# Performance work log

Hardware: AMD Instinct MI355X
Metric: run time of the kernel (lower is better)

## Reference

```python
import jax, jax.numpy as jnp
import numpy as np

N_NODES = 100_000
N_EDGES = 3_200_000
IN_CH = 128
HID = 128


def setup_inputs() -> dict:
    key = jax.random.key(0)
    k1, k2, k3, k4, k5 = jax.random.split(key, 5)
    x = jax.random.normal(k1, (N_NODES, IN_CH), dtype=jnp.float32)
    edge_index = jax.random.randint(k2, (2, N_EDGES), 0, N_NODES, dtype=jnp.int64)
    # GCNConv params: glorot-style weights, zero bias (as in PyG defaults)
    s1 = 1.0 / np.sqrt(IN_CH)
    s2 = 1.0 / np.sqrt(HID)
    W1 = jax.random.uniform(k3, (IN_CH, HID), jnp.float32, -s1, s1)
    b1 = jnp.zeros((HID,), jnp.float32)
    W2 = jax.random.uniform(k4, (HID, HID), jnp.float32, -s2, s2)
    b2 = jnp.zeros((HID,), jnp.float32)
    return {"x": x, "edge_index": edge_index, "W1": W1, "b1": b1, "W2": W2, "b2": b2}


def _gcn_conv(x, src, dst, W, b):
    """PyG GCNConv: add self-loops, symmetric D^-1/2 (A+I) D^-1/2 norm,
    linear transform first, then aggregate, then bias."""
    n = x.shape[0]
    loops = jnp.arange(n, dtype=src.dtype)
    s = jnp.concatenate([src, loops])          # [E+N]
    d = jnp.concatenate([dst, loops])          # [E+N]
    w = jnp.ones(s.shape[0], dtype=x.dtype)    # edge_weight=None -> ones
    deg = jax.ops.segment_sum(w, d, num_segments=n)            # [N]
    dinv = jnp.where(deg > 0, jax.lax.rsqrt(deg), 0.0)         # deg^-1/2
    norm = dinv[s] * w * dinv[d]                                # [E+N]
    xw = x @ W                                                  # [N, H]
    msg = xw[s] * norm[:, None]                                 # [E+N, H] gather
    out = jax.ops.segment_sum(msg, d, num_segments=n)           # [N, H] scatter
    return out + b


def reference(x, edge_index, W1, b1, W2, b2):
    src, dst = edge_index[0], edge_index[1]
    h1 = jax.nn.relu(_gcn_conv(x, src, dst, W1, b1))
    h2 = jax.nn.relu(_gcn_conv(h1, src, dst, W2, b2))
    return jnp.concatenate([h1, h2], axis=1)   # [N, 2*HID]
```

## Files before the change

### kernel.cpp

```cpp
#include <hip/hip_runtime.h>
#include <hip/hip_bf16.h>
#include <stdint.h>

#define NN 100000
#define BSH 9
#define BSZ 512
#define NBUCK 196
#define CAP 24576

static __device__ __forceinline__ float bf_lo(unsigned int u) {
    union { unsigned int i; float f; } c; c.i = u << 16; return c.f;
}
static __device__ __forceinline__ float bf_hi(unsigned int u) {
    union { unsigned int i; float f; } c; c.i = u & 0xffff0000u; return c.f;
}
static __device__ __forceinline__ unsigned short f2bf(float f) {
    union { float f; unsigned int i; } c; c.f = f;
    unsigned int r = (c.i + 0x7fffu + ((c.i >> 16) & 1u)) >> 16;
    return (unsigned short)r;
}

__global__ void k_init(int* __restrict__ gcursor, unsigned int* __restrict__ xwb_row_nn) {
    int i = threadIdx.x;
    if (i < NBUCK) gcursor[i] = i * CAP;
    if (i < 64) xwb_row_nn[i] = 0u;
}

__global__ __launch_bounds__(256) void k_bucket(const int* __restrict__ eb, int E,
                                                int* __restrict__ gcursor,
                                                unsigned int* __restrict__ pairs) {
    __shared__ int hist[NBUCK];
    __shared__ int gbase[NBUCK];
    __shared__ int shflag;
    int t = threadIdx.x;
    if (t < 64) {
        int v = eb[2 * t + 1];
        unsigned long long m = __ballot(v == 0);
        if (t == 0) shflag = (m == ~0ull) ? 1 : 0;
    }
    for (int i = t; i < NBUCK; i += 256) hist[i] = 0;
    __syncthreads();
    int sh = shflag;
    size_t base = (size_t)blockIdx.x * 4096;
    int srcs[16], rank[16], bks[16], dls[16];
#pragma unroll
    for (int k = 0; k < 16; k++) {
        size_t e = base + (size_t)k * 256 + t;
        if (e < (size_t)E) {
            int s = eb[e << sh];
            int d = eb[((size_t)E + e) << sh];
            int b = d >> BSH;
            srcs[k] = s; bks[k] = b; dls[k] = d & (BSZ - 1);
            rank[k] = atomicAdd(&hist[b], 1);
        } else {
            bks[k] = -1;
        }
    }
    __syncthreads();
    for (int i = t; i < NBUCK; i += 256) {
        int c = hist[i];
        gbase[i] = (c > 0) ? atomicAdd(&gcursor[i], c) : 0;
    }
    __syncthreads();
#pragma unroll
    for (int k = 0; k < 16; k++) {
        if (bks[k] >= 0) {
            int pos = gbase[bks[k]] + rank[k];
            if (pos < (bks[k] + 1) * CAP)
                pairs[pos] = ((unsigned int)dls[k] << 17) | (unsigned int)srcs[k];
        }
    }
}

__global__ __launch_bounds__(256) void k_pass2(const unsigned int* __restrict__ pairs,
                                               const int* __restrict__ gcursor,
                                               int* __restrict__ csr, int* __restrict__ ptr,
                                               int* __restrict__ degv, float* __restrict__ dinv) {
    __shared__ int hist2[BSZ * 8];
    __shared__ int cur2[BSZ * 8];
    __shared__ int hist[BSZ];
    __shared__ int lofs[BSZ];
    __shared__ int scanw[256];
    __shared__ int lcsr[CAP];
    int b = blockIdx.x, t = threadIdx.x;
    int base = b * CAP;
    int cnt = gcursor[b] - base;
    if (cnt > CAP) cnt = CAP;
    for (int i = t; i < BSZ * 8; i += 256) hist2[i] = 0;
    __syncthreads();
    for (int i = t; i < cnt; i += 256) {
        unsigned int p = pairs[base + i];
        int key = (int)((p >> 17) << 3) | (int)((p & 0x1FFFFu) >> 14);
        atomicAdd(&hist2[key], 1);
    }
    __syncthreads();
    int dl0 = 2 * t, dl1 = 2 * t + 1;
    int h0 = 0, h1 = 0;
#pragma unroll
    for (int oc = 0; oc < 8; oc++) { h0 += hist2[(dl0 << 3) | oc]; h1 += hist2[(dl1 << 3) | oc]; }
    hist[dl0] = h0; hist[dl1] = h1;
    int a = h0 + h1;
    scanw[t] = a;
    __syncthreads();
    for (int d = 1; d < 256; d <<= 1) {
        int x = (t >= d) ? scanw[t - d] : 0;
        __syncthreads();
        scanw[t] += x;
        __syncthreads();
    }
    int excl = scanw[t] - a;
    lofs[dl0] = excl;
    lofs[dl1] = excl + h0;
    int run = excl;
#pragma unroll
    for (int oc = 0; oc < 8; oc++) { cur2[(dl0 << 3) | oc] = run; run += hist2[(dl0 << 3) | oc]; }
#pragma unroll
    for (int oc = 0; oc < 8; oc++) { cur2[(dl1 << 3) | oc] = run; run += hist2[(dl1 << 3) | oc]; }
    __syncthreads();
    for (int i = t; i < cnt; i += 256) {
        unsigned int p = pairs[base + i];
        int src = (int)(p & 0x1FFFFu);
        int key = (int)((p >> 17) << 3) | (src >> 14);
        int pos = atomicAdd(&cur2[key], 1);
        lcsr[pos] = src;
    }
    __syncthreads();
    for (int i = t; i < cnt; i += 256) csr[base + i] = lcsr[i];
    int n0 = b << BSH;
    for (int g = t; g < BSZ; g += 256) {
        int n = n0 + g;
        if (n < NN) {
            int dg = hist[g];
            degv[n] = dg;
            ptr[n] = base + lofs[g];
            dinv[n] = rsqrtf((float)(dg + 1));
        }
    }
}

__global__ __launch_bounds__(256) void k_gemm(const float* __restrict__ A, int lda,
                                              const float* __restrict__ W,
                                              const float* __restrict__ dinv,
                                              unsigned short* __restrict__ outb, int M) {
    __shared__ float Wl[32 * 128];
    __shared__ float Al[64 * 33];
    int t = threadIdx.x;
    int row0 = blockIdx.x * 64;
    int cg = t & 15, rg = t >> 4;
    int c0 = cg * 8, r0 = rg * 4;
    float acc[4][8];
#pragma unroll
    for (int i = 0; i < 4; i++)
#pragma unroll
        for (int j = 0; j < 8; j++) acc[i][j] = 0.f;

    for (int kb = 0; kb < 4; kb++) {
        __syncthreads();
        const float4* Wg = (const float4*)(W + kb * 32 * 128);
        float4* Wl4 = (float4*)Wl;
#pragma unroll
        for (int i = 0; i < 4; i++) Wl4[t + 256 * i] = Wg[t + 256 * i];
#pragma unroll
        for (int i = 0; i < 2; i++) {
            int idx = t + 256 * i;
            int r = idx >> 3, c4 = idx & 7;
            int grow = row0 + r;
            float4 v = make_float4(0.f, 0.f, 0.f, 0.f);
            if (grow < M) v = *(const float4*)(A + (size_t)grow * lda + kb * 32 + c4 * 4);
            float* dp = &Al[r * 33 + c4 * 4];
            dp[0] = v.x; dp[1] = v.y; dp[2] = v.z; dp[3] = v.w;
        }
        __syncthreads();
#pragma unroll 8
        for (int k = 0; k < 32; k++) {
            float wv[8];
            *(float4*)&wv[0] = *(const float4*)&Wl[k * 128 + c0];
            *(float4*)&wv[4] = *(const float4*)&Wl[k * 128 + c0 + 4];
            float av[4];
#pragma unroll
            for (int i = 0; i < 4; i++) av[i] = Al[(r0 + i) * 33 + k];
#pragma unroll
            for (int i = 0; i < 4; i++)
#pragma unroll
                for (int j = 0; j < 8; j++)
                    acc[i][j] = fmaf(av[i], wv[j], acc[i][j]);
        }
    }
#pragma unroll
    for (int i = 0; i < 4; i++) {
        int grow = row0 + r0 + i;
        if (grow < M) {
            float dv = dinv[grow];
            unsigned int w[4];
#pragma unroll
            for (int j = 0; j < 4; j++)
                w[j] = (unsigned int)f2bf(acc[i][2 * j] * dv) |
                       ((unsigned int)f2bf(acc[i][2 * j + 1] * dv) << 16);
            uint4 pk = make_uint4(w[0], w[1], w[2], w[3]);
            *(uint4*)(outb + (size_t)grow * 128 + c0) = pk;
        }
    }
}

__global__ __launch_bounds__(256) void k_aggr(const unsigned short* __restrict__ xwb,
                                              const int* __restrict__ csr, const int* __restrict__ ptr,
                                              const int* __restrict__ degv,
                                              const float* __restrict__ dinv, const float* __restrict__ bias,
                                              float* __restrict__ outf, int N) {
    int wid = (blockIdx.x * 256 + threadIdx.x) >> 6;
    int lane = threadIdx.x & 63;
    if (wid >= N) return;
    int n = wid;
    int st = ptr[n];
    int en = st + degv[n];
    const unsigned short* xl = xwb + (lane << 1);
    float acc0 = 0.f, acc1 = 0.f;
    for (int j = st; j < en; j += 64) {
        int e = j + lane;
        int sp = (e < en) ? csr[e] : NN;
        int cnt = en - j; if (cnt > 64) cnt = 64;
        int cntr = (cnt + 7) & ~7;
        for (int q = 0; q < cntr; q += 8) {
            int s0 = __shfl(sp, q),     s1 = __shfl(sp, q + 1);
            int s2 = __shfl(sp, q + 2), s3 = __shfl(sp, q + 3);
            int s4 = __shfl(sp, q + 4), s5 = __shfl(sp, q + 5);
            int s6 = __shfl(sp, q + 6), s7 = __shfl(sp, q + 7);
            unsigned int u0 = *(const unsigned int*)(xl + ((size_t)s0 << 7));
            unsigned int u1 = *(const unsigned int*)(xl + ((size_t)s1 << 7));
            unsigned int u2 = *(const unsigned int*)(xl + ((size_t)s2 << 7));
            unsigned int u3 = *(const unsigned int*)(xl + ((size_t)s3 << 7));
            unsigned int u4 = *(const unsigned int*)(xl + ((size_t)s4 << 7));
            unsigned int u5 = *(const unsigned int*)(xl + ((size_t)s5 << 7));
            unsigned int u6 = *(const unsigned int*)(xl + ((size_t)s6 << 7));
            unsigned int u7 = *(const unsigned int*)(xl + ((size_t)s7 << 7));
            acc0 += bf_lo(u0); acc1 += bf_hi(u0);
            acc0 += bf_lo(u1); acc1 += bf_hi(u1);
            acc0 += bf_lo(u2); acc1 += bf_hi(u2);
            acc0 += bf_lo(u3); acc1 += bf_hi(u3);
            acc0 += bf_lo(u4); acc1 += bf_hi(u4);
            acc0 += bf_lo(u5); acc1 += bf_hi(u5);
            acc0 += bf_lo(u6); acc1 += bf_hi(u6);
            acc0 += bf_lo(u7); acc1 += bf_hi(u7);
        }
    }
    {
        unsigned int u = *(const unsigned int*)(xl + ((size_t)n << 7));
        acc0 += bf_lo(u);
        acc1 += bf_hi(u);
    }
    float dn = dinv[n];
    float2 bv = *(const float2*)(bias + (lane << 1));
    float o0 = fmaxf(fmaf(acc0, dn, bv.x), 0.f);
    float o1 = fmaxf(fmaf(acc1, dn, bv.y), 0.f);
    *(float2*)(outf + (size_t)n * 256 + (lane << 1)) = make_float2(o0, o1);
}

extern "C" void kernel_launch(void* const* d_in, const int* in_sizes, int n_in,
                              void* d_out, int out_size, void* d_ws, size_t ws_size,
                              hipStream_t stream) {
    const float* x  = (const float*)d_in[0];
    const int*   eb = (const int*)d_in[1];
    const float* W1 = (const float*)d_in[2];
    const float* b1 = (const float*)d_in[3];
    const float* W2 = (const float*)d_in[4];
    const float* b2 = (const float*)d_in[5];
    float* out = (float*)d_out;

    int E = in_sizes[1] / 2;

    char* w = (char*)d_ws;
    size_t o = 0;
    auto carve = [&](size_t bytes) { char* p = w + o; o += (bytes + 255) & ~(size_t)255; return p; };
    int*   gcursor = (int*)carve((size_t)NBUCK * 4);
    int*   ptr     = (int*)carve((size_t)NN * 4);
    int*   deg     = (int*)carve((size_t)NN * 4);
    float* dinv    = (float*)carve((size_t)NN * 4);
    int*   csr     = (int*)carve((size_t)NBUCK * CAP * 4);
    size_t big = (size_t)(NN + 1) * 128 * 2;
    size_t pb  = (size_t)NBUCK * CAP * 4;
    char* shared_region = carve(big > pb ? big : pb);
    unsigned int*   pairs = (unsigned int*)shared_region;
    unsigned short* xwb   = (unsigned short*)shared_region;
    (void)ws_size;

    int EB4 = (E + 4095) / 4096;
    int GB  = (NN + 63) / 64;
    int AB  = (NN + 3) / 4;

    k_init<<<1, 256, 0, stream>>>(gcursor, (unsigned int*)(xwb + (size_t)NN * 128));
    k_bucket<<<EB4, 256, 0, stream>>>(eb, E, gcursor, pairs);
    k_pass2<<<NBUCK, 256, 0, stream>>>(pairs, gcursor, csr, ptr, deg, dinv);

    k_gemm<<<GB, 256, 0, stream>>>(x, 128, W1, dinv, xwb, NN);
    k_aggr<<<AB, 256, 0, stream>>>(xwb, csr, ptr, deg, dinv, b1, out, NN);

    k_gemm<<<GB, 256, 0, stream>>>(out, 256, W2, dinv, xwb, NN);
    k_aggr<<<AB, 256, 0, stream>>>(xwb, csr, ptr, deg, dinv, b2, out + 128, NN);
}
```

Before: 528.8 us.

## Vectorize aggregation gathers to 16-byte loads and widen pass2 blocks

The aggregation kernel now splits each wavefront into four 16-lane groups. Each group gathers a full 256-byte bf16 row with uint4 loads, two neighbours per step, and the four partial sums are combined with cross-lane xor shuffles. Output is written with nontemporal vector stores. This replaces 4-byte-per-lane gathers with wider loads to cut per-edge memory instructions, at the cost of an extra reduction and idle lanes in the epilogue. Separately, the CSR build kernel runs with 1024 threads per block so the 196 buckets use more parallelism per block.

```diff
diff --git a/kernel.cpp b/kernel.cpp
--- a/kernel.cpp
+++ b/kernel.cpp
@@ -7,6 +7,8 @@
 #define BSZ 512
 #define NBUCK 196
 #define CAP 24576
+
+typedef float vfloat4 __attribute__((ext_vector_type(4)));
 
 static __device__ __forceinline__ float bf_lo(unsigned int u) {
     union { unsigned int i; float f; } c; c.i = u << 16; return c.f;
@@ -72,52 +74,52 @@
     }
 }
 
-__global__ __launch_bounds__(256) void k_pass2(const unsigned int* __restrict__ pairs,
-                                               const int* __restrict__ gcursor,
-                                               int* __restrict__ csr, int* __restrict__ ptr,
-                                               int* __restrict__ degv, float* __restrict__ dinv) {
+__global__ __launch_bounds__(1024) void k_pass2(const unsigned int* __restrict__ pairs,
+                                                const int* __restrict__ gcursor,
+                                                int* __restrict__ csr, int* __restrict__ ptr,
+                                                int* __restrict__ degv, float* __restrict__ dinv) {
     __shared__ int hist2[BSZ * 8];
     __shared__ int cur2[BSZ * 8];
     __shared__ int hist[BSZ];
     __shared__ int lofs[BSZ];
-    __shared__ int scanw[256];
+    __shared__ int scanw[BSZ];
     __shared__ int lcsr[CAP];
     int b = blockIdx.x, t = threadIdx.x;
     int base = b * CAP;
     int cnt = gcursor[b] - base;
     if (cnt > CAP) cnt = CAP;
-    for (int i = t; i < BSZ * 8; i += 256) hist2[i] = 0;
-    __syncthreads();
-    for (int i = t; i < cnt; i += 256) {
+    for (int i = t; i < BSZ * 8; i += 1024) hist2[i] = 0;
+    __syncthreads();
+    for (int i = t; i < cnt; i += 1024) {
         unsigned int p = pairs[base + i];
         int key = (int)((p >> 17) << 3) | (int)((p & 0x1FFFFu) >> 14);
         atomicAdd(&hist2[key], 1);
     }
     __syncthreads();
-    int dl0 = 2 * t, dl1 = 2 * t + 1;
-    int h0 = 0, h1 = 0;
-#pragma unroll
-    for (int oc = 0; oc < 8; oc++) { h0 += hist2[(dl0 << 3) | oc]; h1 += hist2[(dl1 << 3) | oc]; }
-    hist[dl0] = h0; hist[dl1] = h1;
-    int a = h0 + h1;
-    scanw[t] = a;
-    __syncthreads();
-    for (int d = 1; d < 256; d <<= 1) {
-        int x = (t >= d) ? scanw[t - d] : 0;
+    int h = 0;
+    if (t < BSZ) {
+#pragma unroll
+        for (int oc = 0; oc < 8; oc++) h += hist2[(t << 3) | oc];
+        scanw[t] = h;
+        hist[t] = h;
+    }
+    __syncthreads();
+    for (int d = 1; d < BSZ; d <<= 1) {
+        int x = 0;
+        if (t < BSZ && t >= d) x = scanw[t - d];
         __syncthreads();
-        scanw[t] += x;
+        if (t < BSZ) scanw[t] += x;
         __syncthreads();
     }
-    int excl = scanw[t] - a;
-    lofs[dl0] = excl;
-    lofs[dl1] = excl + h0;
-    int run = excl;
-#pragma unroll
-    for (int oc = 0; oc < 8; oc++) { cur2[(dl0 << 3) | oc] = run; run += hist2[(dl0 << 3) | oc]; }
-#pragma unroll
-    for (int oc = 0; oc < 8; oc++) { cur2[(dl1 << 3) | oc] = run; run += hist2[(dl1 << 3) | oc]; }
-    __syncthreads();
-    for (int i = t; i < cnt; i += 256) {
+    if (t < BSZ) {
+        int excl = scanw[t] - h;
+        lofs[t] = excl;
+        int run = excl;
+#pragma unroll
+        for (int oc = 0; oc < 8; oc++) { cur2[(t << 3) | oc] = run; run += hist2[(t << 3) | oc]; }
+    }
+    __syncthreads();
+    for (int i = t; i < cnt; i += 1024) {
         unsigned int p = pairs[base + i];
         int src = (int)(p & 0x1FFFFu);
         int key = (int)((p >> 17) << 3) | (src >> 14);
@@ -125,14 +127,14 @@
         lcsr[pos] = src;
     }
     __syncthreads();
-    for (int i = t; i < cnt; i += 256) csr[base + i] = lcsr[i];
+    for (int i = t; i < cnt; i += 1024) csr[base + i] = lcsr[i];
     int n0 = b << BSH;
-    for (int g = t; g < BSZ; g += 256) {
-        int n = n0 + g;
+    if (t < BSZ) {
+        int n = n0 + t;
         if (n < NN) {
-            int dg = hist[g];
+            int dg = hist[t];
             degv[n] = dg;
-            ptr[n] = base + lofs[g];
+            ptr[n] = base + lofs[t];
             dinv[n] = rsqrtf((float)(dg + 1));
         }
     }
@@ -211,48 +213,61 @@
     int lane = threadIdx.x & 63;
     if (wid >= N) return;
     int n = wid;
+    int g  = lane >> 4;
+    int sl = lane & 15;
     int st = ptr[n];
     int en = st + degv[n];
-    const unsigned short* xl = xwb + (lane << 1);
-    float acc0 = 0.f, acc1 = 0.f;
+    const uint4* xq = (const uint4*)xwb + sl;
+    float acc[8] = {0.f, 0.f, 0.f, 0.f, 0.f, 0.f, 0.f, 0.f};
     for (int j = st; j < en; j += 64) {
         int e = j + lane;
         int sp = (e < en) ? csr[e] : NN;
         int cnt = en - j; if (cnt > 64) cnt = 64;
         int cntr = (cnt + 7) & ~7;
         for (int q = 0; q < cntr; q += 8) {
-            int s0 = __shfl(sp, q),     s1 = __shfl(sp, q + 1);
-            int s2 = __shfl(sp, q + 2), s3 = __shfl(sp, q + 3);
-            int s4 = __shfl(sp, q + 4), s5 = __shfl(sp, q + 5);
-            int s6 = __shfl(sp, q + 6), s7 = __shfl(sp, q + 7);
-            unsigned int u0 = *(const unsigned int*)(xl + ((size_t)s0 << 7));
-            unsigned int u1 = *(const unsigned int*)(xl + ((size_t)s1 << 7));
-            unsigned int u2 = *(const unsigned int*)(xl + ((size_t)s2 << 7));
-            unsigned int u3 = *(const unsigned int*)(xl + ((size_t)s3 << 7));
-            unsigned int u4 = *(const unsigned int*)(xl + ((size_t)s4 << 7));
-            unsigned int u5 = *(const unsigned int*)(xl + ((size_t)s5 << 7));
-            unsigned int u6 = *(const unsigned int*)(xl + ((size_t)s6 << 7));
-            unsigned int u7 = *(const unsigned int*)(xl + ((size_t)s7 << 7));
-            acc0 += bf_lo(u0); acc1 += bf_hi(u0);
-            acc0 += bf_lo(u1); acc1 += bf_hi(u1);
-            acc0 += bf_lo(u2); acc1 += bf_hi(u2);
-            acc0 += bf_lo(u3); acc1 += bf_hi(u3);
-            acc0 += bf_lo(u4); acc1 += bf_hi(u4);
-            acc0 += bf_lo(u5); acc1 += bf_hi(u5);
-            acc0 += bf_lo(u6); acc1 += bf_hi(u6);
-            acc0 += bf_lo(u7); acc1 += bf_hi(u7);
-        }
-    }
-    {
-        unsigned int u = *(const unsigned int*)(xl + ((size_t)n << 7));
-        acc0 += bf_lo(u);
-        acc1 += bf_hi(u);
-    }
-    float dn = dinv[n];
-    float2 bv = *(const float2*)(bias + (lane << 1));
-    float o0 = fmaxf(fmaf(acc0, dn, bv.x), 0.f);
-    float o1 = fmaxf(fmaf(acc1, dn, bv.y), 0.f);
-    *(float2*)(outf + (size_t)n * 256 + (lane << 1)) = make_float2(o0, o1);
+            int s0 = __shfl(sp, q + g);
+            int s1 = __shfl(sp, q + 4 + g);
+            uint4 u0 = xq[(size_t)s0 * 16];
+            uint4 u1 = xq[(size_t)s1 * 16];
+            acc[0] += bf_lo(u0.x); acc[1] += bf_hi(u0.x);
+            acc[2] += bf_lo(u0.y); acc[3] += bf_hi(u0.y);
+            acc[4] += bf_lo(u0.z); acc[5] += bf_hi(u0.z);
+            acc[6] += bf_lo(u0.w); acc[7] += bf_hi(u0.w);
+            acc[0] += bf_lo(u1.x); acc[1] += bf_hi(u1.x);
+            acc[2] += bf_lo(u1.y); acc[3] += bf_hi(u1.y);
+            acc[4] += bf_lo(u1.z); acc[5] += bf_hi(u1.z);
+            acc[6] += bf_lo(u1.w); acc[7] += bf_hi(u1.w);
+        }
+    }
+    if (g == 0) {
+        uint4 u = xq[(size_t)n * 16];
+        acc[0] += bf_lo(u.x); acc[1] += bf_hi(u.x);
+        acc[2] += bf_lo(u.y); acc[3] += bf_hi(u.y);
+        acc[4] += bf_lo(u.z); acc[5] += bf_hi(u.z);
+        acc[6] += bf_lo(u.w); acc[7] += bf_hi(u.w);
+    }
+#pragma unroll
+    for (int i = 0; i < 8; i++) {
+        acc[i] += __shfl_xor(acc[i], 16);
+        acc[i] += __shfl_xor(acc[i], 32);
+    }
+    if (g == 0) {
+        float dn = dinv[n];
+        const float4* bq = (const float4*)bias + 2 * sl;
+        float4 b0 = bq[0], b1 = bq[1];
+        vfloat4 o0, o1;
+        o0.x = fmaxf(fmaf(acc[0], dn, b0.x), 0.f);
+        o0.y = fmaxf(fmaf(acc[1], dn, b0.y), 0.f);
+        o0.z = fmaxf(fmaf(acc[2], dn, b0.z), 0.f);
+        o0.w = fmaxf(fmaf(acc[3], dn, b0.w), 0.f);
+        o1.x = fmaxf(fmaf(acc[4], dn, b1.x), 0.f);
+        o1.y = fmaxf(fmaf(acc[5], dn, b1.y), 0.f);
+        o1.z = fmaxf(fmaf(acc[6], dn, b1.z), 0.f);
+        o1.w = fmaxf(fmaf(acc[7], dn, b1.w), 0.f);
+        vfloat4* op = (vfloat4*)(outf + (size_t)n * 256 + sl * 8);
+        __builtin_nontemporal_store(o0, op);
+        __builtin_nontemporal_store(o1, op + 1);
+    }
 }
 
 extern "C" void kernel_launch(void* const* d_in, const int* in_sizes, int n_in,
@@ -289,7 +304,7 @@
 
     k_init<<<1, 256, 0, stream>>>(gcursor, (unsigned int*)(xwb + (size_t)NN * 128));
     k_bucket<<<EB4, 256, 0, stream>>>(eb, E, gcursor, pairs);
-    k_pass2<<<NBUCK, 256, 0, stream>>>(pairs, gcursor, csr, ptr, deg, dinv);
+    k_pass2<<<NBUCK, 1024, 0, stream>>>(pairs, gcursor, csr, ptr, deg, dinv);
 
     k_gemm<<<GB, 256, 0, stream>>>(x, 128, W1, dinv, xwb, NN);
     k_aggr<<<AB, 256, 0, stream>>>(xwb, csr, ptr, deg, dinv, b1, out, NN);
```

Measured after the change: 513.3 us. -2.9%, faster.
